# Performance work log

Measured on AMD Instinct MI355X. Metric: run time of the kernel, lower is better.

The kernel has to match this reference:

```python
import jax, jax.numpy as jnp
import numpy as np

EPS = 1e-8  # torch.nn.CosineSimilarity default eps


def setup_inputs() -> dict:
    key = jax.random.key(0)
    ks = jax.random.split(key, 6)
    N, M, D = 16384, 2048, 128
    return {
        "query_embed": jax.random.normal(ks[0], (N, D), dtype=jnp.float32),
        "W_t": jax.random.normal(ks[1], (D, D), dtype=jnp.float32) * (1.0 / np.sqrt(D)),
        "b_t": jnp.zeros((D,), dtype=jnp.float32),
        "memory_index_w": jax.random.normal(ks[2], (M, D), dtype=jnp.float32),
        "memory_w": jax.random.normal(ks[3], (M, D), dtype=jnp.float32),
        "W_t2": jax.random.normal(ks[4], (D, 2 * D), dtype=jnp.float32) * (1.0 / np.sqrt(2 * D)),
        "b_t2": jnp.zeros((D,), dtype=jnp.float32),
    }


def reference(query_embed, W_t, b_t, memory_index_w, memory_w, W_t2, b_t2):
    # transform(query_embed): Linear(D, D)
    tq = query_embed @ W_t.T + b_t  # [N, D]
    # cosine similarity vs memory_index embeddings (torch CosineSimilarity, eps clamp on norms)
    tq_n = tq / jnp.clip(jnp.linalg.norm(tq, axis=-1, keepdims=True), EPS)
    mi_n = memory_index_w / jnp.clip(jnp.linalg.norm(memory_index_w, axis=-1, keepdims=True), EPS)
    cos_sim = tq_n @ mi_n.T  # [N, M]
    attn = jax.nn.softmax(cos_sim, axis=1)  # softmax over memory dim
    mem_emb = attn @ memory_w  # [N, D] attention-weighted memory read
    # gating = tanh(transform2(cat(mem_emb, query_embed)))  (dropout = identity in eval)
    gating = jnp.tanh(jnp.concatenate([mem_emb, query_embed], axis=1) @ W_t2.T + b_t2)
    out = (1.0 - gating) * query_embed + gating * mem_emb
    return (out, mem_emb)
```

## Files before the change

kernel.cpp:

```cpp
#include <hip/hip_runtime.h>
#include <hip/hip_bf16.h>

#define NQ 16384
#define MM 2048
#define DD 128

typedef __attribute__((ext_vector_type(8))) short bf16x8;
typedef __attribute__((ext_vector_type(4))) float f32x4;
typedef __attribute__((ext_vector_type(16))) float f32x16;

#define MFMA16(a, b, c) __builtin_amdgcn_mfma_f32_16x16x32_bf16((a), (b), (c), 0, 0, 0)
#define MFMA32(a, b, c) __builtin_amdgcn_mfma_f32_32x32x16_bf16((a), (b), (c), 0, 0, 0)

static __device__ __forceinline__ unsigned short f2bf(float x) {
    union { __hip_bfloat16 h; unsigned short u; } cv;
    cv.h = __float2bfloat16(x);
    return cv.u;
}
static __device__ __forceinline__ unsigned pk2(float a, float b) {
    return (unsigned)f2bf(a) | ((unsigned)f2bf(b) << 16);
}
static __device__ __forceinline__ float bfl(unsigned u) {
    union { unsigned v; float f; } c; c.v = u << 16; return c.f;
}
static __device__ __forceinline__ float bfh(unsigned u) {
    union { unsigned v; float f; } c; c.v = u & 0xffff0000u; return c.f;
}
static __device__ __forceinline__ bf16x8 ldbf8(const unsigned short* p) {
    return *reinterpret_cast<const bf16x8*>(p);
}

union AW { unsigned u[4]; bf16x8 v; };

__global__ __launch_bounds__(256) void k01_prep(const float* __restrict__ miw,
                                                const float* __restrict__ mw,
                                                const float* __restrict__ wt,
                                                const float* __restrict__ wt2,
                                                unsigned short* __restrict__ minnA,
                                                unsigned short* __restrict__ mwB,
                                                unsigned short* __restrict__ wtb,
                                                unsigned short* __restrict__ wt2f) {
    int b = blockIdx.x;
    int t = threadIdx.x;
    if (b >= 64) {
        int i = (b - 64) * 1024 + t * 4;
        if (i < DD * DD) {
            float4 x = *reinterpret_cast<const float4*>(wt + i);
            *reinterpret_cast<uint2*>(wtb + i) = make_uint2(pk2(x.x, x.y), pk2(x.z, x.w));
        } else {
            int j = i - DD * DD;
            float4 x = *reinterpret_cast<const float4*>(wt2 + j);
            int row = j >> 8, col = j & 255;
            unsigned short* dst = wt2f +
                (((((col >> 4) * 4 + (row >> 5)) * 64) + ((col >> 3) & 1) * 32 + (row & 31)) << 3) +
                (col & 7);
            dst[0] = f2bf(x.x); dst[1] = f2bf(x.y); dst[2] = f2bf(x.z); dst[3] = f2bf(x.w);
        }
        return;
    }
    int r = t >> 3;
    int e = t & 7;
    int m = b * 32 + r;

    float v[16];
    float ss = 0.f;
#pragma unroll
    for (int k = 0; k < 4; ++k) {
        float4 x = reinterpret_cast<const float4*>(miw + m * DD + e * 16)[k];
        v[4 * k] = x.x; v[4 * k + 1] = x.y; v[4 * k + 2] = x.z; v[4 * k + 3] = x.w;
        ss += x.x * x.x + x.y * x.y + x.z * x.z + x.w * x.w;
    }
    ss += __shfl_xor(ss, 1); ss += __shfl_xor(ss, 2); ss += __shfl_xor(ss, 4);
    float sc = 1.0f / fmaxf(sqrtf(ss), 1e-8f);

    unsigned u0 = pk2(v[0] * sc, v[1] * sc), u1 = pk2(v[2] * sc, v[3] * sc);
    unsigned u2 = pk2(v[4] * sc, v[5] * sc), u3 = pk2(v[6] * sc, v[7] * sc);
    unsigned u4 = pk2(v[8] * sc, v[9] * sc), u5 = pk2(v[10] * sc, v[11] * sc);
    unsigned u6 = pk2(v[12] * sc, v[13] * sc), u7 = pk2(v[14] * sc, v[15] * sc);
    *reinterpret_cast<uint4*>(minnA + ((((b * 8 + e) * 64) + r) << 3)) = make_uint4(u0, u1, u2, u3);
    *reinterpret_cast<uint4*>(minnA + ((((b * 8 + e) * 64) + 32 + r) << 3)) = make_uint4(u4, u5, u6, u7);

    float w[16];
#pragma unroll
    for (int k = 0; k < 4; ++k) {
        float4 x = reinterpret_cast<const float4*>(mw + m * DD + e * 16)[k];
        w[4 * k] = x.x; w[4 * k + 1] = x.y; w[4 * k + 2] = x.z; w[4 * k + 3] = x.w;
    }
    int kc = r >> 4, hh = (r >> 3) & 1, jj = r & 7;
    unsigned short* base = mwB +
        ((((b * 8 + kc * 4 + (e >> 1)) * 64) + hh * 32 + (e & 1) * 16) << 3) + jj;
#pragma unroll
    for (int u = 0; u < 16; ++u) base[u << 3] = f2bf(w[u]);
}

__global__ __launch_bounds__(512, 2) void k3_fused(const float* __restrict__ query,
                                                   const unsigned short* __restrict__ wtb,
                                                   const float* __restrict__ bt,
                                                   const unsigned short* __restrict__ minnA,
                                                   const unsigned short* __restrict__ mwB,
                                                   const unsigned short* __restrict__ wt2f,
                                                   const float* __restrict__ bt2,
                                                   float* __restrict__ me_out,
                                                   float* __restrict__ out) {
    __shared__ __align__(16) char pool[69632];
    unsigned short* tqm = reinterpret_cast<unsigned short*>(pool + 52224);

    const int lane = threadIdx.x & 63;
    const int wid = threadIdx.x >> 6;
    const int qh = wid >> 2;
    const int mq = wid & 3;
    const int ml = lane & 31;
    const int hi = lane >> 5;
    const int n0 = blockIdx.x * 64;
    const float L2E = 1.44269504088896340736f;

    if (wid < 4) {
        const int nl = lane & 15;
        const int g = lane >> 4;
        const int qb = n0 + 16 * wid;
        AW aq[4];
#pragma unroll
        for (int c = 0; c < 4; ++c) {
            const float* p = query + (qb + nl) * DD + 32 * c + 8 * g;
            float4 x0 = reinterpret_cast<const float4*>(p)[0];
            float4 x1 = reinterpret_cast<const float4*>(p)[1];
            aq[c].u[0] = pk2(x0.x, x0.y); aq[c].u[1] = pk2(x0.z, x0.w);
            aq[c].u[2] = pk2(x1.x, x1.y); aq[c].u[3] = pk2(x1.z, x1.w);
        }
        f32x4 acc[8];
#pragma unroll
        for (int t = 0; t < 8; ++t) acc[t] = (f32x4){0.f, 0.f, 0.f, 0.f};
#pragma unroll
        for (int t = 0; t < 8; ++t)
#pragma unroll
            for (int c = 0; c < 4; ++c) {
                bf16x8 bv = ldbf8(wtb + (16 * t + nl) * DD + 32 * c + 8 * g);
                acc[t] = MFMA16(aq[c].v, bv, acc[t]);
            }
        float ss[4] = {0.f, 0.f, 0.f, 0.f};
#pragma unroll
        for (int t = 0; t < 8; ++t) {
            float bias = bt[16 * t + nl];
#pragma unroll
            for (int r = 0; r < 4; ++r) {
                float vv = acc[t][r] + bias;
                acc[t][r] = vv;
                ss[r] += vv * vv;
            }
        }
#pragma unroll
        for (int r = 0; r < 4; ++r) {
            ss[r] += __shfl_xor(ss[r], 1);
            ss[r] += __shfl_xor(ss[r], 2);
            ss[r] += __shfl_xor(ss[r], 4);
            ss[r] += __shfl_xor(ss[r], 8);
        }
        float scl[4];
#pragma unroll
        for (int r = 0; r < 4; ++r) scl[r] = L2E / fmaxf(sqrtf(ss[r]), 1e-8f);
#pragma unroll
        for (int t = 0; t < 8; ++t)
#pragma unroll
            for (int r = 0; r < 4; ++r)
                tqm[(16 * wid + 4 * g + r) * 136 + 16 * t + nl] = f2bf(acc[t][r] * scl[r]);
    }
    __syncthreads();

    bf16x8 qn[8];
#pragma unroll
    for (int c = 0; c < 8; ++c)
        qn[c] = *reinterpret_cast<const bf16x8*>(&tqm[(32 * qh + ml) * 136 + 16 * c + 8 * hi]);

    const f32x16 zero16 = {0.f,0.f,0.f,0.f,0.f,0.f,0.f,0.f,0.f,0.f,0.f,0.f,0.f,0.f,0.f,0.f};
    f32x16 o[4];
#pragma unroll
    for (int t = 0; t < 4; ++t) o[t] = zero16;
    float den = 0.0f;

    const int mt0 = mq * 16;
    const int rot = blockIdx.x & 15;

    bf16x8 aA[2][8], bw[2][8];
    {
        int ti = mt0 + rot;
#pragma unroll
        for (int c = 0; c < 8; ++c) aA[0][c] = ldbf8(minnA + ((ti * 8 + c) * 64 + lane) * 8);
#pragma unroll
        for (int q = 0; q < 8; ++q) bw[0][q] = ldbf8(mwB + ((ti * 8 + q) * 64 + lane) * 8);
    }

#pragma unroll 2
    for (int it = 0; it < 16; ++it) {
        const int cur = it & 1;
        if (it < 15) {
            int tn = mt0 + ((it + 1 + rot) & 15);
#pragma unroll
            for (int c = 0; c < 8; ++c)
                aA[cur ^ 1][c] = ldbf8(minnA + ((tn * 8 + c) * 64 + lane) * 8);
#pragma unroll
            for (int q = 0; q < 8; ++q)
                bw[cur ^ 1][q] = ldbf8(mwB + ((tn * 8 + q) * 64 + lane) * 8);
        }

        f32x16 sA = zero16, sB = zero16;
#pragma unroll
        for (int c = 0; c < 4; ++c) sA = MFMA32(aA[cur][c], qn[c], sA);
#pragma unroll
        for (int c = 4; c < 8; ++c) sB = MFMA32(aA[cur][c], qn[c], sB);

        float p[16];
#pragma unroll
        for (int r = 0; r < 16; ++r)
            p[r] = __builtin_amdgcn_exp2f(sA[r] + sB[r]);
        {
            float e0 = (p[0] + p[1]) + (p[2] + p[3]);
            float e1 = (p[4] + p[5]) + (p[6] + p[7]);
            float e2 = (p[8] + p[9]) + (p[10] + p[11]);
            float e3 = (p[12] + p[13]) + (p[14] + p[15]);
            den += (e0 + e1) + (e2 + e3);
        }
        unsigned w0 = pk2(p[0], p[1]),   w1 = pk2(p[2], p[3]);
        unsigned w2 = pk2(p[4], p[5]),   w3 = pk2(p[6], p[7]);
        unsigned w4 = pk2(p[8], p[9]),   w5 = pk2(p[10], p[11]);
        unsigned w6 = pk2(p[12], p[13]), w7 = pk2(p[14], p[15]);
        auto r02 = __builtin_amdgcn_permlane32_swap(w0, w2, false, false);
        auto r13 = __builtin_amdgcn_permlane32_swap(w1, w3, false, false);
        auto r46 = __builtin_amdgcn_permlane32_swap(w4, w6, false, false);
        auto r57 = __builtin_amdgcn_permlane32_swap(w5, w7, false, false);
        AW a0, a1;
        a0.u[0] = r02[0]; a0.u[1] = r13[0]; a0.u[2] = r02[1]; a0.u[3] = r13[1];
        a1.u[0] = r46[0]; a1.u[1] = r57[0]; a1.u[2] = r46[1]; a1.u[3] = r57[1];
#pragma unroll
        for (int dt = 0; dt < 4; ++dt) {
            o[dt] = MFMA32(a0.v, bw[cur][dt], o[dt]);
            o[dt] = MFMA32(a1.v, bw[cur][4 + dt], o[dt]);
        }
    }

    if (mq >= 1) {
        char* dst = pool + (qh * 3 + (mq - 1)) * 8704 + lane * 136;
#pragma unroll
        for (int t = 0; t < 4; ++t) {
            unsigned u[8];
#pragma unroll
            for (int k = 0; k < 8; ++k) u[k] = pk2(o[t][2 * k], o[t][2 * k + 1]);
            *reinterpret_cast<uint4*>(dst + t * 32) = make_uint4(u[0], u[1], u[2], u[3]);
            *reinterpret_cast<uint4*>(dst + t * 32 + 16) = make_uint4(u[4], u[5], u[6], u[7]);
        }
        *reinterpret_cast<float*>(dst + 128) = den;
    }
    __syncthreads();
    if (mq == 0) {
        for (int s = 0; s < 3; ++s) {
            const char* src = pool + (qh * 3 + s) * 8704 + lane * 136;
#pragma unroll
            for (int t = 0; t < 4; ++t) {
                uint4 ua = *reinterpret_cast<const uint4*>(src + t * 32);
                uint4 ub = *reinterpret_cast<const uint4*>(src + t * 32 + 16);
                unsigned u[8] = {ua.x, ua.y, ua.z, ua.w, ub.x, ub.y, ub.z, ub.w};
#pragma unroll
                for (int k = 0; k < 8; ++k) {
                    o[t][2 * k] += bfl(u[k]);
                    o[t][2 * k + 1] += bfh(u[k]);
                }
            }
            den += *reinterpret_cast<const float*>(src + 128);
        }
        den += __shfl_xor(den, 32);
        float invd = 1.0f / den;
        float inv[16];
#pragma unroll
        for (int r = 0; r < 16; ++r)
            inv[r] = __shfl(invd, (r & 3) + 8 * (r >> 2) + 4 * hi);
#pragma unroll
        for (int t = 0; t < 4; ++t)
#pragma unroll
            for (int r = 0; r < 16; ++r) {
                int row = 32 * qh + (r & 3) + 8 * (r >> 2) + 4 * hi;
                float me = o[t][r] * inv[r];
                me_out[(n0 + row) * DD + 32 * t + ml] = me;
                tqm[row * 136 + 32 * t + ml] = f2bf(me);
            }
    }
    __syncthreads();

    {
        const int qg = wid >> 2;
        const int dt = wid & 3;
        f32x16 g = zero16;
#pragma unroll
        for (int c = 0; c < 8; ++c) {
            bf16x8 av = *reinterpret_cast<const bf16x8*>(
                &tqm[(32 * qg + ml) * 136 + 16 * c + 8 * hi]);
            bf16x8 bv = ldbf8(wt2f + ((c * 4 + dt) * 64 + lane) * 8);
            g = MFMA32(av, bv, g);
        }
#pragma unroll
        for (int c = 8; c < 16; ++c) {
            const float* p = query + (n0 + 32 * qg + ml) * DD + 16 * (c - 8) + 8 * hi;
            float4 x0 = reinterpret_cast<const float4*>(p)[0];
            float4 x1 = reinterpret_cast<const float4*>(p)[1];
            AW av;
            av.u[0] = pk2(x0.x, x0.y); av.u[1] = pk2(x0.z, x0.w);
            av.u[2] = pk2(x1.x, x1.y); av.u[3] = pk2(x1.z, x1.w);
            bf16x8 bv = ldbf8(wt2f + ((c * 4 + dt) * 64 + lane) * 8);
            g = MFMA32(av.v, bv, g);
        }
        const float TWO_L2E = 2.88539008177792681472f;
        const int d = 32 * dt + ml;
        const float bias = bt2[d];
#pragma unroll
        for (int r = 0; r < 16; ++r) {
            int row = 32 * qg + (r & 3) + 8 * (r >> 2) + 4 * hi;
            float x = g[r] + bias;
            float gt = 1.0f - 2.0f / (__builtin_amdgcn_exp2f(x * TWO_L2E) + 1.0f);
            float qv = query[(n0 + row) * DD + d];
            float mv = bfl(tqm[row * 136 + d]);
            out[(n0 + row) * DD + d] = qv + gt * (mv - qv);
        }
    }
}

extern "C" void kernel_launch(void* const* d_in, const int* in_sizes, int n_in,
                              void* d_out, int out_size, void* d_ws, size_t ws_size,
                              hipStream_t stream) {
    const float* query = (const float*)d_in[0];
    const float* wt    = (const float*)d_in[1];
    const float* bt    = (const float*)d_in[2];
    const float* miw   = (const float*)d_in[3];
    const float* mw    = (const float*)d_in[4];
    const float* wt2   = (const float*)d_in[5];
    const float* bt2   = (const float*)d_in[6];

    float* out    = (float*)d_out;
    float* me_out = out + (size_t)NQ * DD;

    unsigned short* minnA = (unsigned short*)d_ws;
    unsigned short* mwB   = minnA + (size_t)MM * DD;
    unsigned short* wtb   = mwB + (size_t)MM * DD;
    unsigned short* wt2f  = wtb + (size_t)DD * DD;

    k01_prep<<<112, 256, 0, stream>>>(miw, mw, wt, wt2, minnA, mwB, wtb, wt2f);
    k3_fused<<<NQ / 64, 512, 0, stream>>>(query, wtb, bt, minnA, mwB, wt2f, bt2,
                                          me_out, out);
}
```

Measured before the change: 47.58 us.

## Switch attention GEMMs from bf16 to fp8 MFMA with per-iteration barrier

Converts the normalized memory-index keys, memory values, normalized queries and softmax probabilities to fp8 and runs both attention matmuls with the 32x32x16 fp8 MFMA instead of bf16. This halves the global and register footprint of the streamed K/V tiles and the probability-repack work, aiming to cut memory traffic and register pressure in the main loop. It also adds a workgroup barrier each iteration, likely to keep waves in lockstep for cache sharing, plus extra syncthreads around LDS reuse. fp8 precision on keys, values and probabilities risks accuracy loss against the fp32 reference.

New measurement: 50.50 us. +6.1%, slower.

```diff
diff --git a/kernel.cpp b/kernel.cpp
--- a/kernel.cpp
+++ b/kernel.cpp
@@ -11,6 +11,7 @@
 
 #define MFMA16(a, b, c) __builtin_amdgcn_mfma_f32_16x16x32_bf16((a), (b), (c), 0, 0, 0)
 #define MFMA32(a, b, c) __builtin_amdgcn_mfma_f32_32x32x16_bf16((a), (b), (c), 0, 0, 0)
+#define MFMA32F8(a, b, c) __builtin_amdgcn_mfma_f32_32x32x16_fp8_fp8((a), (b), (c), 0, 0, 0)
 
 static __device__ __forceinline__ unsigned short f2bf(float x) {
     union { __hip_bfloat16 h; unsigned short u; } cv;
@@ -29,6 +30,14 @@
 static __device__ __forceinline__ bf16x8 ldbf8(const unsigned short* p) {
     return *reinterpret_cast<const bf16x8*>(p);
 }
+static __device__ __forceinline__ unsigned pk4f8(float a, float b, float c, float d) {
+    int v = __builtin_amdgcn_cvt_pk_fp8_f32(a, b, 0, false);
+    v = __builtin_amdgcn_cvt_pk_fp8_f32(c, d, v, true);
+    return (unsigned)v;
+}
+static __device__ __forceinline__ unsigned char f8b(float x) {
+    return (unsigned char)(__builtin_amdgcn_cvt_pk_fp8_f32(x, x, 0, false) & 0xff);
+}
 
 union AW { unsigned u[4]; bf16x8 v; };
 
@@ -36,8 +45,8 @@
                                                 const float* __restrict__ mw,
                                                 const float* __restrict__ wt,
                                                 const float* __restrict__ wt2,
-                                                unsigned short* __restrict__ minnA,
-                                                unsigned short* __restrict__ mwB,
+                                                unsigned char* __restrict__ minnA8,
+                                                unsigned char* __restrict__ mwB8,
                                                 unsigned short* __restrict__ wtb,
                                                 unsigned short* __restrict__ wt2f) {
     int b = blockIdx.x;
@@ -73,12 +82,14 @@
     ss += __shfl_xor(ss, 1); ss += __shfl_xor(ss, 2); ss += __shfl_xor(ss, 4);
     float sc = 1.0f / fmaxf(sqrtf(ss), 1e-8f);
 
-    unsigned u0 = pk2(v[0] * sc, v[1] * sc), u1 = pk2(v[2] * sc, v[3] * sc);
-    unsigned u2 = pk2(v[4] * sc, v[5] * sc), u3 = pk2(v[6] * sc, v[7] * sc);
-    unsigned u4 = pk2(v[8] * sc, v[9] * sc), u5 = pk2(v[10] * sc, v[11] * sc);
-    unsigned u6 = pk2(v[12] * sc, v[13] * sc), u7 = pk2(v[14] * sc, v[15] * sc);
-    *reinterpret_cast<uint4*>(minnA + ((((b * 8 + e) * 64) + r) << 3)) = make_uint4(u0, u1, u2, u3);
-    *reinterpret_cast<uint4*>(minnA + ((((b * 8 + e) * 64) + 32 + r) << 3)) = make_uint4(u4, u5, u6, u7);
+    {
+        unsigned lo0 = pk4f8(v[0] * sc, v[1] * sc, v[2] * sc, v[3] * sc);
+        unsigned lo1 = pk4f8(v[4] * sc, v[5] * sc, v[6] * sc, v[7] * sc);
+        unsigned hi0 = pk4f8(v[8] * sc, v[9] * sc, v[10] * sc, v[11] * sc);
+        unsigned hi1 = pk4f8(v[12] * sc, v[13] * sc, v[14] * sc, v[15] * sc);
+        *reinterpret_cast<uint2*>(minnA8 + ((((b * 8 + e) * 64) + r) << 3)) = make_uint2(lo0, lo1);
+        *reinterpret_cast<uint2*>(minnA8 + ((((b * 8 + e) * 64) + 32 + r) << 3)) = make_uint2(hi0, hi1);
+    }
 
     float w[16];
 #pragma unroll
@@ -87,22 +98,23 @@
         w[4 * k] = x.x; w[4 * k + 1] = x.y; w[4 * k + 2] = x.z; w[4 * k + 3] = x.w;
     }
     int kc = r >> 4, hh = (r >> 3) & 1, jj = r & 7;
-    unsigned short* base = mwB +
+    unsigned char* base = mwB8 +
         ((((b * 8 + kc * 4 + (e >> 1)) * 64) + hh * 32 + (e & 1) * 16) << 3) + jj;
 #pragma unroll
-    for (int u = 0; u < 16; ++u) base[u << 3] = f2bf(w[u]);
+    for (int u = 0; u < 16; ++u) base[u << 3] = f8b(w[u]);
 }
 
 __global__ __launch_bounds__(512, 2) void k3_fused(const float* __restrict__ query,
                                                    const unsigned short* __restrict__ wtb,
                                                    const float* __restrict__ bt,
-                                                   const unsigned short* __restrict__ minnA,
-                                                   const unsigned short* __restrict__ mwB,
+                                                   const unsigned char* __restrict__ minnA8,
+                                                   const unsigned char* __restrict__ mwB8,
                                                    const unsigned short* __restrict__ wt2f,
                                                    const float* __restrict__ bt2,
                                                    float* __restrict__ me_out,
                                                    float* __restrict__ out) {
     __shared__ __align__(16) char pool[69632];
+    unsigned char* qf8 = reinterpret_cast<unsigned char*>(pool);
     unsigned short* tqm = reinterpret_cast<unsigned short*>(pool + 52224);
 
     const int lane = threadIdx.x & 63;
@@ -162,14 +174,15 @@
         for (int t = 0; t < 8; ++t)
 #pragma unroll
             for (int r = 0; r < 4; ++r)
-                tqm[(16 * wid + 4 * g + r) * 136 + 16 * t + nl] = f2bf(acc[t][r] * scl[r]);
-    }
-    __syncthreads();
-
-    bf16x8 qn[8];
+                qf8[(16 * wid + 4 * g + r) * 128 + 16 * t + nl] = f8b(acc[t][r] * scl[r]);
+    }
+    __syncthreads();
+
+    long qn8[8];
 #pragma unroll
     for (int c = 0; c < 8; ++c)
-        qn[c] = *reinterpret_cast<const bf16x8*>(&tqm[(32 * qh + ml) * 136 + 16 * c + 8 * hi]);
+        qn8[c] = *reinterpret_cast<const long*>(qf8 + (32 * qh + ml) * 128 + 16 * c + 8 * hi);
+    __syncthreads();
 
     const f32x16 zero16 = {0.f,0.f,0.f,0.f,0.f,0.f,0.f,0.f,0.f,0.f,0.f,0.f,0.f,0.f,0.f,0.f};
     f32x16 o[4];
@@ -180,33 +193,38 @@
     const int mt0 = mq * 16;
     const int rot = blockIdx.x & 15;
 
-    bf16x8 aA[2][8], bw[2][8];
+    long aA8[2][8], bw8[2][8];
     {
         int ti = mt0 + rot;
 #pragma unroll
-        for (int c = 0; c < 8; ++c) aA[0][c] = ldbf8(minnA + ((ti * 8 + c) * 64 + lane) * 8);
-#pragma unroll
-        for (int q = 0; q < 8; ++q) bw[0][q] = ldbf8(mwB + ((ti * 8 + q) * 64 + lane) * 8);
+        for (int c = 0; c < 8; ++c)
+            aA8[0][c] = *reinterpret_cast<const long*>(minnA8 + (((ti * 8 + c) * 64 + lane) << 3));
+#pragma unroll
+        for (int q = 0; q < 8; ++q)
+            bw8[0][q] = *reinterpret_cast<const long*>(mwB8 + (((ti * 8 + q) * 64 + lane) << 3));
     }
 
 #pragma unroll 2
     for (int it = 0; it < 16; ++it) {
         const int cur = it & 1;
+        __builtin_amdgcn_s_barrier();
         if (it < 15) {
             int tn = mt0 + ((it + 1 + rot) & 15);
 #pragma unroll
             for (int c = 0; c < 8; ++c)
-                aA[cur ^ 1][c] = ldbf8(minnA + ((tn * 8 + c) * 64 + lane) * 8);
+                aA8[cur ^ 1][c] = *reinterpret_cast<const long*>(
+                    minnA8 + (((tn * 8 + c) * 64 + lane) << 3));
 #pragma unroll
             for (int q = 0; q < 8; ++q)
-                bw[cur ^ 1][q] = ldbf8(mwB + ((tn * 8 + q) * 64 + lane) * 8);
+                bw8[cur ^ 1][q] = *reinterpret_cast<const long*>(
+                    mwB8 + (((tn * 8 + q) * 64 + lane) << 3));
         }
 
         f32x16 sA = zero16, sB = zero16;
 #pragma unroll
-        for (int c = 0; c < 4; ++c) sA = MFMA32(aA[cur][c], qn[c], sA);
-#pragma unroll
-        for (int c = 4; c < 8; ++c) sB = MFMA32(aA[cur][c], qn[c], sB);
+        for (int c = 0; c < 4; ++c) sA = MFMA32F8(aA8[cur][c], qn8[c], sA);
+#pragma unroll
+        for (int c = 4; c < 8; ++c) sB = MFMA32F8(aA8[cur][c], qn8[c], sB);
 
         float p[16];
 #pragma unroll
@@ -219,24 +237,22 @@
             float e3 = (p[12] + p[13]) + (p[14] + p[15]);
             den += (e0 + e1) + (e2 + e3);
         }
-        unsigned w0 = pk2(p[0], p[1]),   w1 = pk2(p[2], p[3]);
-        unsigned w2 = pk2(p[4], p[5]),   w3 = pk2(p[6], p[7]);
-        unsigned w4 = pk2(p[8], p[9]),   w5 = pk2(p[10], p[11]);
-        unsigned w6 = pk2(p[12], p[13]), w7 = pk2(p[14], p[15]);
-        auto r02 = __builtin_amdgcn_permlane32_swap(w0, w2, false, false);
-        auto r13 = __builtin_amdgcn_permlane32_swap(w1, w3, false, false);
-        auto r46 = __builtin_amdgcn_permlane32_swap(w4, w6, false, false);
-        auto r57 = __builtin_amdgcn_permlane32_swap(w5, w7, false, false);
-        AW a0, a1;
-        a0.u[0] = r02[0]; a0.u[1] = r13[0]; a0.u[2] = r02[1]; a0.u[3] = r13[1];
-        a1.u[0] = r46[0]; a1.u[1] = r57[0]; a1.u[2] = r46[1]; a1.u[3] = r57[1];
+        unsigned u0 = pk4f8(p[0], p[1], p[2], p[3]);
+        unsigned u1 = pk4f8(p[4], p[5], p[6], p[7]);
+        unsigned u2 = pk4f8(p[8], p[9], p[10], p[11]);
+        unsigned u3 = pk4f8(p[12], p[13], p[14], p[15]);
+        auto s01 = __builtin_amdgcn_permlane32_swap(u0, u1, false, false);
+        auto s23 = __builtin_amdgcn_permlane32_swap(u2, u3, false, false);
+        long aP0 = (long)(((unsigned long long)(unsigned)s01[1] << 32) | (unsigned)s01[0]);
+        long aP1 = (long)(((unsigned long long)(unsigned)s23[1] << 32) | (unsigned)s23[0]);
 #pragma unroll
         for (int dt = 0; dt < 4; ++dt) {
-            o[dt] = MFMA32(a0.v, bw[cur][dt], o[dt]);
-            o[dt] = MFMA32(a1.v, bw[cur][4 + dt], o[dt]);
-        }
-    }
-
+            o[dt] = MFMA32F8(aP0, bw8[cur][dt], o[dt]);
+            o[dt] = MFMA32F8(aP1, bw8[cur][4 + dt], o[dt]);
+        }
+    }
+
+    __syncthreads();
     if (mq >= 1) {
         char* dst = pool + (qh * 3 + (mq - 1)) * 8704 + lane * 136;
 #pragma unroll
@@ -335,12 +351,12 @@
     float* out    = (float*)d_out;
     float* me_out = out + (size_t)NQ * DD;
 
-    unsigned short* minnA = (unsigned short*)d_ws;
-    unsigned short* mwB   = minnA + (size_t)MM * DD;
-    unsigned short* wtb   = mwB + (size_t)MM * DD;
+    unsigned char* minnA8 = (unsigned char*)d_ws;
+    unsigned char* mwB8   = minnA8 + (size_t)MM * DD;
+    unsigned short* wtb   = (unsigned short*)(mwB8 + (size_t)MM * DD);
     unsigned short* wt2f  = wtb + (size_t)DD * DD;
 
-    k01_prep<<<112, 256, 0, stream>>>(miw, mw, wt, wt2, minnA, mwB, wtb, wt2f);
-    k3_fused<<<NQ / 64, 512, 0, stream>>>(query, wtb, bt, minnA, mwB, wt2f, bt2,
+    k01_prep<<<112, 256, 0, stream>>>(miw, mw, wt, wt2, minnA8, mwB8, wtb, wt2f);
+    k3_fused<<<NQ / 64, 512, 0, stream>>>(query, wtb, bt, minnA8, mwB8, wt2f, bt2,
                                           me_out, out);
 }
```
